# Performance work log

Hardware: AMD Instinct MI355X
Metric: run time of the kernel (lower is better)

The kernel has to match this reference:

```python
import jax, jax.numpy as jnp
import numpy as np

NUM_HEADS = 12

def setup_inputs() -> dict:
    key = jax.random.key(0)
    ks = jax.random.split(key, 5)
    dim = 768
    x = jax.random.normal(ks[0], (2, 64, 64, dim), dtype=jnp.float32)
    qkv_w = jax.random.normal(ks[1], (3 * dim, dim), dtype=jnp.float32) * 0.02
    qkv_b = jax.random.normal(ks[2], (3 * dim,), dtype=jnp.float32) * 0.02
    proj_w = jax.random.normal(ks[3], (dim, dim), dtype=jnp.float32) * 0.02
    proj_b = jax.random.normal(ks[4], (dim,), dtype=jnp.float32) * 0.02
    return {"x": x, "qkv_w": qkv_w, "qkv_b": qkv_b, "proj_w": proj_w, "proj_b": proj_b}

def reference(x, qkv_w, qkv_b, proj_w, proj_b):
    B, H, W, C = x.shape
    N = H * W
    nh = NUM_HEADS
    hd = C // nh
    scale = hd ** -0.5
    # qkv linear: (B,H,W,3C)
    qkv = jnp.einsum('bhwc,dc->bhwd', x, qkv_w) + qkv_b
    qkv = qkv.reshape(B, N, 3, nh, hd).transpose(2, 0, 3, 1, 4)  # (3,B,nh,N,hd)
    q, k, v = qkv[0], qkv[1], qkv[2]
    # (B,nh,N,N) attention scores, stable softmax
    attn = jax.nn.softmax(jnp.einsum('bhqd,bhkd->bhqk', q * scale, k), axis=-1)
    out = jnp.einsum('bhqk,bhkd->bhqd', attn, v)  # (B,nh,N,hd)
    out = out.transpose(0, 2, 1, 3).reshape(B, N, C)
    # Source quirk: for 4D input the output stays (B, N, C) after proj.
    return jnp.einsum('bnc,dc->bnd', out, proj_w) + proj_b
```

## Files before the change

### kernel.cpp

```cpp
#include <hip/hip_runtime.h>
#include <hip/hip_bf16.h>

#define LOG2E 1.44269504088896340736f

typedef __attribute__((ext_vector_type(8))) short short8;
typedef __attribute__((ext_vector_type(2))) float f32x2;
typedef __attribute__((ext_vector_type(4))) float f32x4;
typedef __attribute__((ext_vector_type(16))) float f32x16;

__device__ __forceinline__ unsigned short f2bf(float f) {
    unsigned int u = __float_as_uint(f);
    u += 0x7fffu + ((u >> 16) & 1u);
    return (unsigned short)(u >> 16);
}

__device__ __forceinline__ unsigned cvt_pk_bf16(float a, float b) {
    unsigned r;
    asm("v_cvt_pk_bf16_f32 %0, %1, %2" : "=v"(r) : "v"(a), "v"(b));
    return r;
}

__device__ __forceinline__ float fast_exp2(float x) {
    float r;
    asm("v_exp_f32 %0, %1" : "=v"(r) : "v"(x));
    return r;
}

__device__ __forceinline__ void gl_lds16(const unsigned short* g, unsigned short* l) {
    __builtin_amdgcn_global_load_lds(
        (const __attribute__((address_space(1))) unsigned int*)g,
        (__attribute__((address_space(3))) unsigned int*)l, 16, 0, 0);
}

__global__ void cvt_swz(const float* __restrict__ in,
                        unsigned short* __restrict__ out, int n8) {
    int stride = gridDim.x * blockDim.x;
    for (int i = blockIdx.x * blockDim.x + threadIdx.x; i < n8; i += stride) {
        int flat = i * 8;
        int row = flat / 768;
        int col = flat - row * 768;
        float4 v0 = ((const float4*)(in + flat))[0];
        float4 v1 = ((const float4*)(in + flat))[1];
        union { unsigned short u[8]; short8 v; } o;
        o.u[0] = f2bf(v0.x); o.u[1] = f2bf(v0.y);
        o.u[2] = f2bf(v0.z); o.u[3] = f2bf(v0.w);
        o.u[4] = f2bf(v1.x); o.u[5] = f2bf(v1.y);
        o.u[6] = f2bf(v1.z); o.u[7] = f2bf(v1.w);
        int c = (col & 63) ^ ((row & 7) << 3);
        *(short8*)(out + (size_t)row * 768 + (col & ~63) + c) = o.v;
    }
}

template <int EPI, int BN>
__global__ __launch_bounds__(256, BN == 64 ? 3 : 2)
void gemm_bt(const unsigned short* __restrict__ A,
             const unsigned short* __restrict__ B,
             const float* __restrict__ bias,
             void* __restrict__ Cout,
             int M, int N, int K) {
    __shared__ unsigned short As[2][8192];
    __shared__ unsigned short Bs[2][BN * 64];
    constexpr int NB = BN / 32;

    const int tid  = threadIdx.x;
    const int wave = tid >> 6, lane = tid & 63;
    const int fr = lane & 15, fg = lane >> 4;
    const int wm = (wave >> 1) * 64, wn = (wave & 1) * (BN / 2);
    const int m0 = blockIdx.y * 128, n0 = blockIdx.x * BN;
    const int sr = lane >> 3, ss = lane & 7;

    f32x4 acc[4][NB];
#pragma unroll
    for (int m = 0; m < 4; m++)
#pragma unroll
        for (int n = 0; n < NB; n++) acc[m][n] = (f32x4){0.f, 0.f, 0.f, 0.f};

    const int NT = K >> 6;

#define GEMM_STAGE(buf, k0)                                                     \
    {                                                                           \
        _Pragma("unroll")                                                       \
        for (int c = 0; c < 4; c++) {                                           \
            int rr = (c * 4 + wave) * 8 + sr;                                   \
            gl_lds16(A + (size_t)(m0 + rr) * K + (k0) + ss * 8,                 \
                     &As[buf][(c * 4 + wave) * 512]);                           \
        }                                                                       \
        _Pragma("unroll")                                                       \
        for (int c = 0; c < NB; c++) {                                          \
            int rr = (c * 4 + wave) * 8 + sr;                                   \
            gl_lds16(B + (size_t)(n0 + rr) * K + (k0) + ss * 8,                 \
                     &Bs[buf][(c * 4 + wave) * 512]);                           \
        }                                                                       \
    }

    GEMM_STAGE(0, 0)

    for (int t = 0; t < NT; t++) {
        __syncthreads();
        if (t + 1 < NT) GEMM_STAGE((t + 1) & 1, (t + 1) << 6)
        const unsigned short* ab = As[t & 1];
        const unsigned short* bb = Bs[t & 1];
        __builtin_amdgcn_s_setprio(1);
#pragma unroll
        for (int ks = 0; ks < 2; ks++) {
            short8 af[4], bfr[NB];
#pragma unroll
            for (int m = 0; m < 4; m++)
                af[m] = *(const short8*)&ab[(wm + m * 16 + fr) * 64 +
                                            (((ks * 4 + fg) ^ (fr & 7)) << 3)];
#pragma unroll
            for (int n = 0; n < NB; n++)
                bfr[n] = *(const short8*)&bb[(wn + n * 16 + fr) * 64 +
                                             (((ks * 4 + fg) ^ (fr & 7)) << 3)];
#pragma unroll
            for (int m = 0; m < 4; m++)
#pragma unroll
                for (int n = 0; n < NB; n++)
                    acc[m][n] = __builtin_amdgcn_mfma_f32_16x16x32_bf16(
                        af[m], bfr[n], acc[m][n], 0, 0, 0);
        }
        __builtin_amdgcn_s_setprio(0);
    }
#undef GEMM_STAGE

#pragma unroll
    for (int m = 0; m < 4; m++) {
#pragma unroll
        for (int n = 0; n < NB; n++) {
            int gn = n0 + wn + n * 16 + fr;
            float bv = bias[gn];
#pragma unroll
            for (int j = 0; j < 4; j++) {
                int gm = m0 + wm + m * 16 + fg * 4 + j;
                float v = acc[m][n][j] + bv;
                if (EPI == 0) {
                    int which = gn / 768, rem = gn % 768;
                    int h = rem >> 6, d = rem & 63;
                    int b = gm >> 12, nn = gm & 4095;
                    if (which == 0) v *= (0.125f * LOG2E);
                    unsigned short* o = (unsigned short*)Cout;
                    size_t base = (((size_t)which * 2 + b) * 12 + h) * 262144;
                    if (which == 2)
                        o[base + (size_t)d * 4096 + nn] = f2bf(v);
                    else
                        o[base + (size_t)nn * 64 + d] = f2bf(v);
                } else {
                    float* o = (float*)Cout;
                    o[(size_t)gm * 768 + gn] = v;
                }
            }
        }
    }
}

__device__ __forceinline__ void attn_iter(
    short8 (&rK)[2], short8 (&rV)[2], int kt,
    const unsigned short* __restrict__ kh,
    const unsigned short* __restrict__ vht,
    int r, int sg, int l31, int l31p, int hh,
    unsigned short (&Ks)[64][72], unsigned short (&Vt)[64][72],
    const short8 (&qf)[4],
    float& mrow, f32x16& accA, f32x16& accB, f32x2 (&ls)[8]) {
    __syncthreads();
#pragma unroll
    for (int c = 0; c < 2; c++) {
        int kr = r + c * 32;
        *(short8*)&Ks[kr][sg * 8] = rK[c];
        *(short8*)&Vt[kr][sg * 8] = rV[c];
    }
    if (kt + 2 < 64) {
        const unsigned short* kb = kh + (size_t)(kt + 2) * 4096;
#pragma unroll
        for (int c = 0; c < 2; c++) {
            int kr = r + c * 32;
            rK[c] = *(const short8*)(kb + kr * 64 + sg * 8);
            rV[c] = *(const short8*)(vht + (size_t)kr * 4096 + (kt + 2) * 64 + sg * 8);
        }
    }
    __syncthreads();

    f32x16 s0 = (f32x16)0.f, s1 = (f32x16)0.f;
    __builtin_amdgcn_s_setprio(1);
#pragma unroll
    for (int ks = 0; ks < 4; ks++) {
        short8 kf0 = *(const short8*)&Ks[l31p][ks * 16 + hh * 8];
        short8 kf1 = *(const short8*)&Ks[32 + l31p][ks * 16 + hh * 8];
        s0 = __builtin_amdgcn_mfma_f32_32x32x16_bf16(kf0, qf[ks], s0, 0, 0, 0);
        s1 = __builtin_amdgcn_mfma_f32_32x32x16_bf16(kf1, qf[ks], s1, 0, 0, 0);
    }
    __builtin_amdgcn_s_setprio(0);

    union F16 { f32x16 v; f32x2 p[8]; float f[16]; };
    F16 a, b2;
    a.v = s0; b2.v = s1;

    f32x2 m2[8];
#pragma unroll
    for (int i = 0; i < 8; i++) m2[i] = __builtin_elementwise_max(a.p[i], b2.p[i]);
#pragma unroll
    for (int i = 0; i < 4; i++) m2[i] = __builtin_elementwise_max(m2[i], m2[i + 4]);
    m2[0] = __builtin_elementwise_max(m2[0], m2[2]);
    m2[1] = __builtin_elementwise_max(m2[1], m2[3]);
    m2[0] = __builtin_elementwise_max(m2[0], m2[1]);
    float mx = fmaxf(m2[0][0], m2[0][1]);
    mx = fmaxf(mx, __shfl_xor(mx, 32));

    if (!__all(mx - mrow <= 8.0f)) {
        float mnew = fmaxf(mrow, mx);
        float corr = fast_exp2(mrow - mnew);
        mrow = mnew;
        f32x2 c2 = {corr, corr};
#pragma unroll
        for (int i = 0; i < 16; i++) { accA[i] *= corr; accB[i] *= corr; }
#pragma unroll
        for (int i = 0; i < 8; i++) ls[i] *= c2;
    }

    f32x2 nm = {-mrow, -mrow};
#pragma unroll
    for (int i = 0; i < 8; i++) { a.p[i] += nm; b2.p[i] += nm; }
#pragma unroll
    for (int i = 0; i < 16; i++) {
        a.f[i]  = fast_exp2(a.f[i]);
        b2.f[i] = fast_exp2(b2.f[i]);
    }
#pragma unroll
    for (int i = 0; i < 8; i++) ls[i] += a.p[i] + b2.p[i];

    short8 pf[4];
    {
        union { unsigned w[4]; short8 v; } up;
        up.w[0] = cvt_pk_bf16(a.f[0], a.f[1]);   up.w[1] = cvt_pk_bf16(a.f[2], a.f[3]);
        up.w[2] = cvt_pk_bf16(a.f[4], a.f[5]);   up.w[3] = cvt_pk_bf16(a.f[6], a.f[7]);
        pf[0] = up.v;
        up.w[0] = cvt_pk_bf16(a.f[8], a.f[9]);   up.w[1] = cvt_pk_bf16(a.f[10], a.f[11]);
        up.w[2] = cvt_pk_bf16(a.f[12], a.f[13]); up.w[3] = cvt_pk_bf16(a.f[14], a.f[15]);
        pf[1] = up.v;
        up.w[0] = cvt_pk_bf16(b2.f[0], b2.f[1]);   up.w[1] = cvt_pk_bf16(b2.f[2], b2.f[3]);
        up.w[2] = cvt_pk_bf16(b2.f[4], b2.f[5]);   up.w[3] = cvt_pk_bf16(b2.f[6], b2.f[7]);
        pf[2] = up.v;
        up.w[0] = cvt_pk_bf16(b2.f[8], b2.f[9]);   up.w[1] = cvt_pk_bf16(b2.f[10], b2.f[11]);
        up.w[2] = cvt_pk_bf16(b2.f[12], b2.f[13]); up.w[3] = cvt_pk_bf16(b2.f[14], b2.f[15]);
        pf[3] = up.v;
    }

    __builtin_amdgcn_s_setprio(1);
#pragma unroll
    for (int ks2 = 0; ks2 < 4; ks2++) {
        short8 vf0 = *(const short8*)&Vt[l31][ks2 * 16 + hh * 8];
        short8 vf1 = *(const short8*)&Vt[32 + l31][ks2 * 16 + hh * 8];
        accA = __builtin_amdgcn_mfma_f32_32x32x16_bf16(vf0, pf[ks2], accA, 0, 0, 0);
        accB = __builtin_amdgcn_mfma_f32_32x32x16_bf16(vf1, pf[ks2], accB, 0, 0, 0);
    }
    __builtin_amdgcn_s_setprio(0);
}

__global__ __launch_bounds__(256, 3)
void attn_fwd(const unsigned short* __restrict__ qkv,
              unsigned short* __restrict__ outp) {
    __shared__ unsigned short Ks[64][72];
    __shared__ unsigned short Vt[64][72];

    const int tid  = threadIdx.x;
    const int wave = tid >> 6, lane = tid & 63;
    const int l31 = lane & 31, hh = lane >> 5;
    const int l31p = (l31 & 0x13) | ((l31 & 4) << 1) | ((l31 & 8) >> 1);

    const int qt = blockIdx.x;
    const int bh = blockIdx.y;
    const int b = bh / 12, h = bh % 12;

    const size_t headsz = (size_t)4096 * 64;
    const unsigned short* qh  = qkv + ((size_t)b * 12 + h) * headsz;
    const unsigned short* kh  = qkv + ((size_t)(2 + b) * 12 + h) * headsz;
    const unsigned short* vht = qkv + ((size_t)(4 + b) * 12 + h) * headsz;

    const int qw = qt * 128 + wave * 32;
    const int gq = qw + l31;

    short8 qf[4];
#pragma unroll
    for (int ks = 0; ks < 4; ks++)
        qf[ks] = *(const short8*)(qh + (size_t)gq * 64 + ks * 16 + hh * 8);

    float mrow = -1e30f;
    f32x16 accA = (f32x16)0.f, accB = (f32x16)0.f;
    f32x2 ls[8];
#pragma unroll
    for (int i = 0; i < 8; i++) ls[i] = (f32x2){0.f, 0.f};

    const int r = tid >> 3, sg = tid & 7;

    short8 rKa[2], rVa[2], rKb[2], rVb[2];
#pragma unroll
    for (int c = 0; c < 2; c++) {
        int kr = r + c * 32;
        rKa[c] = *(const short8*)(kh + (size_t)kr * 64 + sg * 8);
        rVa[c] = *(const short8*)(vht + (size_t)kr * 4096 + sg * 8);
        rKb[c] = *(const short8*)(kh + (size_t)4096 + kr * 64 + sg * 8);
        rVb[c] = *(const short8*)(vht + (size_t)kr * 4096 + 64 + sg * 8);
    }

    for (int kt = 0; kt < 64; kt += 2) {
        attn_iter(rKa, rVa, kt,     kh, vht, r, sg, l31, l31p, hh,
                  Ks, Vt, qf, mrow, accA, accB, ls);
        attn_iter(rKb, rVb, kt + 1, kh, vht, r, sg, l31, l31p, hh,
                  Ks, Vt, qf, mrow, accA, accB, ls);
    }

#pragma unroll
    for (int w = 4; w >= 1; w >>= 1)
#pragma unroll
        for (int i = 0; i < 4; i++)
            if (i < w) ls[i] += ls[i + w];
    float lr = ls[0][0] + ls[0][1];
    lr += __shfl_xor(lr, 32);
    float inv = 1.0f / lr;

    size_t rowoff = (size_t)(b * 4096 + gq) * 768 + h * 64;
    int sw = l31 & 7;
#pragma unroll
    for (int g = 0; g < 4; g++) {
        ushort4 o;
        o.x = f2bf(accA[4 * g + 0] * inv);
        o.y = f2bf(accA[4 * g + 1] * inv);
        o.z = f2bf(accA[4 * g + 2] * inv);
        o.w = f2bf(accA[4 * g + 3] * inv);
        *(ushort4*)(outp + rowoff + ((g ^ sw) * 8) + hh * 4) = o;
        o.x = f2bf(accB[4 * g + 0] * inv);
        o.y = f2bf(accB[4 * g + 1] * inv);
        o.z = f2bf(accB[4 * g + 2] * inv);
        o.w = f2bf(accB[4 * g + 3] * inv);
        *(ushort4*)(outp + rowoff + (((4 + g) ^ sw) * 8) + hh * 4) = o;
    }
}

extern "C" void kernel_launch(void* const* d_in, const int* in_sizes, int n_in,
                              void* d_out, int out_size, void* d_ws, size_t ws_size,
                              hipStream_t stream) {
    const float* x      = (const float*)d_in[0];
    const float* qkv_w  = (const float*)d_in[1];
    const float* qkv_b  = (const float*)d_in[2];
    const float* proj_w = (const float*)d_in[3];
    const float* proj_b = (const float*)d_in[4];
    float* out = (float*)d_out;

    char* ws = (char*)d_ws;
    unsigned short* x_bf    = (unsigned short*)(ws);
    unsigned short* w1_bf   = (unsigned short*)(ws + 12582912);
    unsigned short* w2_bf   = (unsigned short*)(ws + 16121856);
    unsigned short* qkv_sep = (unsigned short*)(ws + 17301504);
    unsigned short* att     = (unsigned short*)(ws + 55050240);

    cvt_swz<<<2048, 256, 0, stream>>>(x,      x_bf,  6291456 / 8);
    cvt_swz<<<864,  256, 0, stream>>>(qkv_w,  w1_bf, 1769472 / 8);
    cvt_swz<<<288,  256, 0, stream>>>(proj_w, w2_bf,  589824 / 8);

    gemm_bt<0, 128><<<dim3(18, 64), 256, 0, stream>>>(x_bf, w1_bf, qkv_b, qkv_sep,
                                                      8192, 2304, 768);

    attn_fwd<<<dim3(32, 24), 256, 0, stream>>>(qkv_sep, att);

    gemm_bt<1, 64><<<dim3(12, 64), 256, 0, stream>>>(att, w2_bf, proj_b, out,
                                                     8192, 768, 768);
}
```

Measured before the change: 228.3 us.

## Double-buffer K/V shared tiles to drop one barrier per attention iteration

Splits the K and V shared-memory tiles into two ping-pong buffers. Each iteration computes on the current buffer while writing the next tile from registers into the other, and a single barrier at the end of the iteration replaces the two barriers before. The prologue preloads the first tile into LDS and shifts the register prefetch one tile further ahead. This doubles LDS use per block, which could limit occupancy at 3 blocks per CU.

New measurement: 259.7 us. 13.8% more time.

```diff
diff --git a/kernel.cpp b/kernel.cpp
--- a/kernel.cpp
+++ b/kernel.cpp
@@ -158,37 +158,39 @@
     const unsigned short* __restrict__ kh,
     const unsigned short* __restrict__ vht,
     int r, int sg, int l31, int l31p, int hh,
-    unsigned short (&Ks)[64][72], unsigned short (&Vt)[64][72],
+    const unsigned short* curK, const unsigned short* curV,
+    unsigned short* nxtK, unsigned short* nxtV,
     const short8 (&qf)[4],
     float& mrow, f32x16& accA, f32x16& accB, f32x2 (&ls)[8]) {
-    __syncthreads();
-#pragma unroll
-    for (int c = 0; c < 2; c++) {
-        int kr = r + c * 32;
-        *(short8*)&Ks[kr][sg * 8] = rK[c];
-        *(short8*)&Vt[kr][sg * 8] = rV[c];
-    }
-    if (kt + 2 < 64) {
-        const unsigned short* kb = kh + (size_t)(kt + 2) * 4096;
+
+    f32x16 s0 = (f32x16)0.f, s1 = (f32x16)0.f;
+    __builtin_amdgcn_s_setprio(1);
+#pragma unroll
+    for (int ks = 0; ks < 4; ks++) {
+        short8 kf0 = *(const short8*)&curK[l31p * 72 + ks * 16 + hh * 8];
+        short8 kf1 = *(const short8*)&curK[(32 + l31p) * 72 + ks * 16 + hh * 8];
+        s0 = __builtin_amdgcn_mfma_f32_32x32x16_bf16(kf0, qf[ks], s0, 0, 0, 0);
+        s1 = __builtin_amdgcn_mfma_f32_32x32x16_bf16(kf1, qf[ks], s1, 0, 0, 0);
+    }
+    __builtin_amdgcn_s_setprio(0);
+
+    if (kt + 1 < 64) {
+#pragma unroll
+        for (int c = 0; c < 2; c++) {
+            int kr = r + c * 32;
+            *(short8*)&nxtK[kr * 72 + sg * 8] = rK[c];
+            *(short8*)&nxtV[kr * 72 + sg * 8] = rV[c];
+        }
+    }
+    if (kt + 3 < 64) {
+        const unsigned short* kb = kh + (size_t)(kt + 3) * 4096;
 #pragma unroll
         for (int c = 0; c < 2; c++) {
             int kr = r + c * 32;
             rK[c] = *(const short8*)(kb + kr * 64 + sg * 8);
-            rV[c] = *(const short8*)(vht + (size_t)kr * 4096 + (kt + 2) * 64 + sg * 8);
+            rV[c] = *(const short8*)(vht + (size_t)kr * 4096 + (kt + 3) * 64 + sg * 8);
         }
     }
-    __syncthreads();
-
-    f32x16 s0 = (f32x16)0.f, s1 = (f32x16)0.f;
-    __builtin_amdgcn_s_setprio(1);
-#pragma unroll
-    for (int ks = 0; ks < 4; ks++) {
-        short8 kf0 = *(const short8*)&Ks[l31p][ks * 16 + hh * 8];
-        short8 kf1 = *(const short8*)&Ks[32 + l31p][ks * 16 + hh * 8];
-        s0 = __builtin_amdgcn_mfma_f32_32x32x16_bf16(kf0, qf[ks], s0, 0, 0, 0);
-        s1 = __builtin_amdgcn_mfma_f32_32x32x16_bf16(kf1, qf[ks], s1, 0, 0, 0);
-    }
-    __builtin_amdgcn_s_setprio(0);
 
     union F16 { f32x16 v; f32x2 p[8]; float f[16]; };
     F16 a, b2;
@@ -247,19 +249,21 @@
     __builtin_amdgcn_s_setprio(1);
 #pragma unroll
     for (int ks2 = 0; ks2 < 4; ks2++) {
-        short8 vf0 = *(const short8*)&Vt[l31][ks2 * 16 + hh * 8];
-        short8 vf1 = *(const short8*)&Vt[32 + l31][ks2 * 16 + hh * 8];
+        short8 vf0 = *(const short8*)&curV[l31 * 72 + ks2 * 16 + hh * 8];
+        short8 vf1 = *(const short8*)&curV[(32 + l31) * 72 + ks2 * 16 + hh * 8];
         accA = __builtin_amdgcn_mfma_f32_32x32x16_bf16(vf0, pf[ks2], accA, 0, 0, 0);
         accB = __builtin_amdgcn_mfma_f32_32x32x16_bf16(vf1, pf[ks2], accB, 0, 0, 0);
     }
     __builtin_amdgcn_s_setprio(0);
+
+    __syncthreads();
 }
 
 __global__ __launch_bounds__(256, 3)
 void attn_fwd(const unsigned short* __restrict__ qkv,
               unsigned short* __restrict__ outp) {
-    __shared__ unsigned short Ks[64][72];
-    __shared__ unsigned short Vt[64][72];
+    __shared__ unsigned short Ks0[64 * 72], Vt0[64 * 72];
+    __shared__ unsigned short Ks1[64 * 72], Vt1[64 * 72];
 
     const int tid  = threadIdx.x;
     const int wave = tid >> 6, lane = tid & 63;
@@ -300,12 +304,25 @@
         rKb[c] = *(const short8*)(kh + (size_t)4096 + kr * 64 + sg * 8);
         rVb[c] = *(const short8*)(vht + (size_t)kr * 4096 + 64 + sg * 8);
     }
+#pragma unroll
+    for (int c = 0; c < 2; c++) {
+        int kr = r + c * 32;
+        *(short8*)&Ks0[kr * 72 + sg * 8] = rKa[c];
+        *(short8*)&Vt0[kr * 72 + sg * 8] = rVa[c];
+    }
+#pragma unroll
+    for (int c = 0; c < 2; c++) {
+        int kr = r + c * 32;
+        rKa[c] = *(const short8*)(kh + (size_t)2 * 4096 + kr * 64 + sg * 8);
+        rVa[c] = *(const short8*)(vht + (size_t)kr * 4096 + 128 + sg * 8);
+    }
+    __syncthreads();
 
     for (int kt = 0; kt < 64; kt += 2) {
-        attn_iter(rKa, rVa, kt,     kh, vht, r, sg, l31, l31p, hh,
-                  Ks, Vt, qf, mrow, accA, accB, ls);
-        attn_iter(rKb, rVb, kt + 1, kh, vht, r, sg, l31, l31p, hh,
-                  Ks, Vt, qf, mrow, accA, accB, ls);
+        attn_iter(rKb, rVb, kt,     kh, vht, r, sg, l31, l31p, hh,
+                  Ks0, Vt0, Ks1, Vt1, qf, mrow, accA, accB, ls);
+        attn_iter(rKa, rVa, kt + 1, kh, vht, r, sg, l31, l31p, hh,
+                  Ks1, Vt1, Ks0, Vt0, qf, mrow, accA, accB, ls);
     }
 
 #pragma unroll
```
